# Optimization experiments

Measured on AMD Instinct MI355X. Metric: run time of the kernel, lower is better.

Reference implementation:

```python
import jax, jax.numpy as jnp
import numpy as np

B, T, D = 1, 2048, 4096
H, G = 32, 8
HD = D // H          # 128
REP = H // G         # 4
KV_DIM = 2 * HD * G  # 2048


def setup_inputs() -> dict:
    key = jax.random.key(0)
    k0, k1, k2, k3 = jax.random.split(key, 4)
    x = jax.random.normal(k0, (B, T, D), dtype=jnp.float32)
    Wq = jax.random.normal(k1, (D, D), dtype=jnp.float32) * 0.02
    Wkv = jax.random.normal(k2, (D, KV_DIM), dtype=jnp.float32) * 0.02
    Wo = jax.random.normal(k3, (D, D), dtype=jnp.float32) * 0.02
    bo = jnp.zeros((D,), dtype=jnp.float32)
    return {"x": x, "Wq": Wq, "Wkv": Wkv, "Wo": Wo, "bo": bo}


def reference(x, Wq, Wkv, Wo, bo):
    b, t, d = x.shape
    # projections (qkv_bias=False)
    q = jnp.dot(x, Wq).reshape(b, t, H, HD).transpose(0, 2, 1, 3)        # (b,H,t,hd)
    kv = jnp.dot(x, Wkv).reshape(b, t, G, 2, HD).transpose(2, 3, 0, 1, 4)  # (G,2,b,t,hd)
    k, v = kv[:, 0], kv[:, 1]                                             # (G,b,t,hd)
    # faithful to torch: unsqueeze+repeat then flat view(b, H, t, hd)
    k = jnp.broadcast_to(k[:, :, None], (G, b, REP, t, HD)).reshape(b, H, t, HD)
    v = jnp.broadcast_to(v[:, :, None], (G, b, REP, t, HD)).reshape(b, H, t, HD)
    # attention: mask then scale, matching original order
    scores = jnp.einsum('bhqd,bhkd->bhqk', q, k)                          # (b,H,t,t)
    causal = jnp.triu(jnp.ones((t, t), dtype=bool), 1)
    scores = jnp.where(causal[None, None], -jnp.inf, scores)
    weights = jax.nn.softmax(scores * (1.0 / HD ** 0.5), axis=-1)
    ctx = jnp.einsum('bhqk,bhkd->bhqd', weights, v)                       # (b,H,t,hd)
    ctx = ctx.transpose(0, 2, 1, 3).reshape(b, t, d)
    return jnp.dot(ctx, Wo) + bo
```

## Files before the change

### kernel.cpp

```cpp
#include <hip/hip_runtime.h>

#define T_SEQ 2048
#define D_MODEL 4096
#define NH 32
#define NG 8
#define HD 128

typedef unsigned short u16;
typedef __bf16 bf16x8 __attribute__((ext_vector_type(8)));
typedef float f32x4 __attribute__((ext_vector_type(4)));

#define AS1 __attribute__((address_space(1)))
#define AS3 __attribute__((address_space(3)))

__device__ __forceinline__ void async_cp16(const u16* g, u16* l) {
  __builtin_amdgcn_global_load_lds((AS1 void*)g, (AS3 void*)l, 16, 0, 0);
}

__device__ __forceinline__ u16 f2bf(float f){
  union { float f; unsigned x; } v; v.f = f;
  unsigned r = v.x + 0x7FFFu + ((v.x >> 16) & 1u);
  return (u16)(r >> 16);
}

__global__ __launch_bounds__(256) void cvt_k(const float* __restrict__ in,
                                             u16* __restrict__ out, int n4)
{
  int i = blockIdx.x * 256 + threadIdx.x;
  if (i >= n4) return;
  float4 v = *(const float4*)&in[(size_t)i * 4];
  short4 o;
  o.x = (short)f2bf(v.x); o.y = (short)f2bf(v.y);
  o.z = (short)f2bf(v.z); o.w = (short)f2bf(v.w);
  *(short4*)&out[(size_t)i * 4] = o;
}

__global__ __launch_bounds__(256) void transpose_k(const float* __restrict__ in,
                                                   u16* __restrict__ out, int R, int C)
{
  __shared__ __align__(16) u16 tile[32][36];
  int c0 = blockIdx.x * 32, r0 = blockIdx.y * 32;
  int t = threadIdx.x;
  int lr = t >> 3, lc = (t & 7) * 4;
  float4 v4 = *(const float4*)&in[(size_t)(r0 + lr) * C + c0 + lc];
  tile[lr][lc + 0] = f2bf(v4.x);
  tile[lr][lc + 1] = f2bf(v4.y);
  tile[lr][lc + 2] = f2bf(v4.z);
  tile[lr][lc + 3] = f2bf(v4.w);
  __syncthreads();
  short4 v;
  v.x = (short)tile[lc + 0][lr];
  v.y = (short)tile[lc + 1][lr];
  v.z = (short)tile[lc + 2][lr];
  v.w = (short)tile[lc + 3][lr];
  *(short4*)&out[(size_t)(c0 + lr) * R + r0 + lc] = v;
}

template<int MODE>
__global__ __launch_bounds__(256) void gemm_k(
    const u16* __restrict__ A, const u16* __restrict__ BT,
    u16* __restrict__ Cout, u16* __restrict__ Kout, u16* __restrict__ Vout,
    float* __restrict__ Fout, const float* __restrict__ bias, int K, int N)
{
  __shared__ __align__(16) u16 sA[2 * 128 * 64];
  __shared__ __align__(16) u16 sB[2 * 128 * 64];
  const int t = threadIdx.x;
  const int lane = t & 63, wave = t >> 6;
  const int quad = lane >> 4, lm = lane & 15;
  const int wm = wave >> 1, wn = wave & 1;
  const int m0 = blockIdx.y * 128, n0 = blockIdx.x * 128;
  const int ntk = K >> 6;
  const f32x4 fzero = {0.f, 0.f, 0.f, 0.f};

  const int sr_sub = lane >> 3;
  const int sgl = (lane & 7) ^ sr_sub;

  f32x4 acc[4][4];
  #pragma unroll
  for (int i = 0; i < 4; i++)
    #pragma unroll
    for (int j = 0; j < 4; j++) acc[i][j] = fzero;

  auto stage = [&](int td) {
    const int k0 = td << 6;
    u16* dA = sA + (td & 1) * (128 * 64);
    u16* dB = sB + (td & 1) * (128 * 64);
    #pragma unroll
    for (int c = 0; c < 4; c++) {
      int r = c * 32 + wave * 8 + sr_sub;
      async_cp16(&A [(size_t)(m0 + r) * K + k0 + sgl * 8], &dA[(c * 256 + wave * 64) * 8]);
      async_cp16(&BT[(size_t)(n0 + r) * K + k0 + sgl * 8], &dB[(c * 256 + wave * 64) * 8]);
    }
  };

  stage(0);
  stage(1);

  for (int ti = 0; ti < ntk; ++ti) {
    if (ti + 1 < ntk) { asm volatile("s_waitcnt vmcnt(8)" ::: "memory"); }
    else             { asm volatile("s_waitcnt vmcnt(0)" ::: "memory"); }
    __builtin_amdgcn_s_barrier();
    asm volatile("" ::: "memory");

    const u16* cA = sA + (ti & 1) * (128 * 64);
    const u16* cB = sB + (ti & 1) * (128 * 64);

    __builtin_amdgcn_s_setprio(1);
    #pragma unroll
    for (int kb = 0; kb < 2; kb++) {
      bf16x8 af[4], bfr[4];
      #pragma unroll
      for (int mt = 0; mt < 4; mt++) {
        int row = wm * 64 + mt * 16 + lm;
        af[mt] = *(const bf16x8*)&cA[row * 64 + (((kb * 4 + quad) ^ (lm & 7)) * 8)];
      }
      #pragma unroll
      for (int nt = 0; nt < 4; nt++) {
        int row = wn * 64 + nt * 16 + lm;
        bfr[nt] = *(const bf16x8*)&cB[row * 64 + (((kb * 4 + quad) ^ (lm & 7)) * 8)];
      }
      #pragma unroll
      for (int mt = 0; mt < 4; mt++)
        #pragma unroll
        for (int nt = 0; nt < 4; nt++)
          acc[mt][nt] = __builtin_amdgcn_mfma_f32_16x16x32_bf16(af[mt], bfr[nt], acc[mt][nt], 0, 0, 0);
    }
    __builtin_amdgcn_s_setprio(0);

    __builtin_amdgcn_s_barrier();
    asm volatile("" ::: "memory");
    if (ti + 2 < ntk) stage(ti + 2);
  }

  #pragma unroll
  for (int mt = 0; mt < 4; mt++) {
    #pragma unroll
    for (int nt = 0; nt < 4; nt++) {
      int gcol = n0 + wn * 64 + nt * 16 + lm;
      int grow0 = m0 + wm * 64 + mt * 16 + quad * 4;
      if (MODE == 0) {
        #pragma unroll
        for (int r = 0; r < 4; r++)
          Cout[(size_t)(grow0 + r) * N + gcol] = f2bf(acc[mt][nt][r]);
      } else if (MODE == 1) {
        int g = gcol >> 8, s = (gcol >> 7) & 1, hd = gcol & 127;
        if (s) {
          short4 pv;
          pv.x = (short)f2bf(acc[mt][nt][0]);
          pv.y = (short)f2bf(acc[mt][nt][1]);
          pv.z = (short)f2bf(acc[mt][nt][2]);
          pv.w = (short)f2bf(acc[mt][nt][3]);
          *(short4*)&Vout[((size_t)g * HD + hd) * T_SEQ + grow0] = pv;
        } else {
          #pragma unroll
          for (int r = 0; r < 4; r++)
            Kout[((size_t)g * T_SEQ + grow0 + r) * HD + hd] = f2bf(acc[mt][nt][r]);
        }
      } else {
        #pragma unroll
        for (int r = 0; r < 4; r++)
          Fout[(size_t)(grow0 + r) * N + gcol] = acc[mt][nt][r] + bias[gcol];
      }
    }
  }
}

__global__ __launch_bounds__(256) void attn_k(
    const u16* __restrict__ Q, const u16* __restrict__ Kb,
    const u16* __restrict__ Vt, u16* __restrict__ ctx)
{
  __shared__ __align__(16) u16 sK[2 * 64 * 128];
  __shared__ __align__(16) u16 sV[2 * 128 * 64];
  __shared__ __align__(16) u16 sP[4 * 16 * 72];
  const int t = threadIdx.x;
  const int lane = t & 63, wave = t >> 6;
  const int quad = lane >> 4, lm = lane & 15;

  const int id = blockIdx.x + gridDim.x * blockIdx.y;
  const int g = id & 7;
  const int idx = id >> 3;
  const int h = g * 4 + (idx & 3);
  const int q0 = (31 - (idx >> 2)) * 64;
  const int nt = (q0 >> 6) + 1;

  const float scale = 0.088388347648318447f;
  const float C1 = scale * 1.4426950408889634f;
  const float C2 = -14.0f * 1.4426950408889634f;
  const f32x4 fzero = {0.f, 0.f, 0.f, 0.f};

  bf16x8 aq[4];
  {
    const u16* qp = Q + (size_t)(q0 + wave * 16 + lm) * D_MODEL + h * HD + quad * 8;
    #pragma unroll
    for (int kb = 0; kb < 4; kb++) aq[kb] = *(const bf16x8*)(qp + kb * 32);
  }
  bf16x8 bones;
  #pragma unroll
  for (int i = 0; i < 8; i++) bones[i] = (__bf16)1.0f;

  f32x4 o[8];
  #pragma unroll
  for (int i = 0; i < 8; i++) o[i] = fzero;
  f32x4 lacc = fzero;

  const u16* Kg = Kb + (size_t)g * T_SEQ * HD;
  const u16* Vg = Vt + (size_t)g * HD * T_SEQ;
  u16* sPw = sP + wave * 16 * 72;

  const int k_r_sub = lane >> 4;
  const int v_r_sub = lane >> 3;
  const int v_gl = (lane & 7) ^ v_r_sub;

  auto stage = [&](int td) {
    const int kv0 = td << 6;
    u16* dK = sK + (td & 1) * (64 * 128);
    u16* dV = sV + (td & 1) * (128 * 64);
    #pragma unroll
    for (int c = 0; c < 4; c++) {
      int rk = c * 16 + wave * 4 + k_r_sub;
      int kgl = (lane & 15) ^ (rk & 7);
      async_cp16(&Kg[(size_t)(kv0 + rk) * HD + kgl * 8], &dK[(c * 256 + wave * 64) * 8]);
      int rv = c * 32 + wave * 8 + v_r_sub;
      async_cp16(&Vg[(size_t)rv * T_SEQ + kv0 + v_gl * 8], &dV[(c * 256 + wave * 64) * 8]);
    }
  };

  stage(0);
  if (nt > 1) stage(1);

  for (int ti = 0; ti < nt; ++ti) {
    if (ti + 1 < nt) { asm volatile("s_waitcnt vmcnt(8)" ::: "memory"); }
    else             { asm volatile("s_waitcnt vmcnt(0)" ::: "memory"); }
    __builtin_amdgcn_s_barrier();
    asm volatile("" ::: "memory");

    const u16* cK = sK + (ti & 1) * (64 * 128);
    const u16* cV = sV + (ti & 1) * (128 * 64);
    const int kv0 = ti << 6;

    f32x4 s[4];
    __builtin_amdgcn_s_setprio(1);
    #pragma unroll
    for (int nt4 = 0; nt4 < 4; nt4++) {
      s[nt4] = fzero;
      #pragma unroll
      for (int kb = 0; kb < 4; kb++) {
        int row = nt4 * 16 + lm;
        bf16x8 bk = *(const bf16x8*)&cK[row * 128 + (((kb * 4 + quad) ^ (lm & 7)) * 8)];
        s[nt4] = __builtin_amdgcn_mfma_f32_16x16x32_bf16(aq[kb], bk, s[nt4], 0, 0, 0);
      }
    }
    __builtin_amdgcn_s_setprio(0);

    if (ti == nt - 1) {
      #pragma unroll
      for (int r = 0; r < 4; r++) {
        int qr = q0 + wave * 16 + quad * 4 + r;
        #pragma unroll
        for (int nt4 = 0; nt4 < 4; nt4++) {
          int kvc = kv0 + nt4 * 16 + lm;
          float p = exp2f(fmaf(s[nt4][r], C1, C2));
          p = (kvc > qr) ? 0.f : p;
          sPw[(quad * 4 + r) * 72 + nt4 * 16 + lm] = f2bf(p);
        }
      }
    } else {
      #pragma unroll
      for (int r = 0; r < 4; r++) {
        #pragma unroll
        for (int nt4 = 0; nt4 < 4; nt4++) {
          float p = exp2f(fmaf(s[nt4][r], C1, C2));
          sPw[(quad * 4 + r) * 72 + nt4 * 16 + lm] = f2bf(p);
        }
      }
    }

    __builtin_amdgcn_s_setprio(1);
    #pragma unroll
    for (int kb2 = 0; kb2 < 2; kb2++) {
      bf16x8 ap = *(const bf16x8*)&sPw[lm * 72 + kb2 * 32 + quad * 8];
      lacc = __builtin_amdgcn_mfma_f32_16x16x32_bf16(ap, bones, lacc, 0, 0, 0);
      #pragma unroll
      for (int n8 = 0; n8 < 8; n8++) {
        int row = n8 * 16 + lm;
        bf16x8 bv = *(const bf16x8*)&cV[row * 64 + (((kb2 * 4 + quad) ^ (lm & 7)) * 8)];
        o[n8] = __builtin_amdgcn_mfma_f32_16x16x32_bf16(ap, bv, o[n8], 0, 0, 0);
      }
    }
    __builtin_amdgcn_s_setprio(0);

    __builtin_amdgcn_s_barrier();
    asm volatile("" ::: "memory");
    if (ti + 2 < nt) stage(ti + 2);
  }

  #pragma unroll
  for (int r = 0; r < 4; r++) {
    float inv = 1.f / lacc[r];
    #pragma unroll
    for (int n8 = 0; n8 < 8; n8++) {
      ctx[(size_t)(q0 + wave * 16 + quad * 4 + r) * D_MODEL + h * HD + n8 * 16 + lm]
          = f2bf(o[n8][r] * inv);
    }
  }
}

extern "C" void kernel_launch(void* const* d_in, const int* in_sizes, int n_in,
                              void* d_out, int out_size, void* d_ws, size_t ws_size,
                              hipStream_t stream)
{
  const float* x   = (const float*)d_in[0];
  const float* Wq  = (const float*)d_in[1];
  const float* Wkv = (const float*)d_in[2];
  const float* Wo  = (const float*)d_in[3];
  const float* bo  = (const float*)d_in[4];
  float* out = (float*)d_out;

  char* ws = (char*)d_ws;
  const size_t SZ_T   = 33554432;
  const size_t SZ_ACT = 16777216;
  const size_t SZ_KV  = 4194304;
  u16* Tb = (u16*)(ws);
  u16* Xb = (u16*)(ws + SZ_T);
  u16* Qb = (u16*)(ws + SZ_T + SZ_ACT);
  u16* Kb = (u16*)(ws + SZ_T + 2 * SZ_ACT);
  u16* Vt = (u16*)(ws + SZ_T + 2 * SZ_ACT + SZ_KV);
  u16* Cx = Xb;

  cvt_k<<<dim3(8192, 1, 1), 256, 0, stream>>>(x, Xb, 2097152);
  transpose_k<<<dim3(128, 128, 1), 256, 0, stream>>>(Wq, Tb, 4096, 4096);
  gemm_k<0><<<dim3(32, 16, 1), 256, 0, stream>>>(Xb, Tb, Qb, nullptr, nullptr, nullptr, nullptr, 4096, 4096);
  transpose_k<<<dim3(64, 128, 1), 256, 0, stream>>>(Wkv, Tb, 4096, 2048);
  gemm_k<1><<<dim3(16, 16, 1), 256, 0, stream>>>(Xb, Tb, nullptr, Kb, Vt, nullptr, nullptr, 4096, 2048);
  attn_k<<<dim3(32, 32, 1), 256, 0, stream>>>(Qb, Kb, Vt, Cx);
  transpose_k<<<dim3(128, 128, 1), 256, 0, stream>>>(Wo, Tb, 4096, 4096);
  gemm_k<2><<<dim3(32, 16, 1), 256, 0, stream>>>(Cx, Tb, nullptr, nullptr, nullptr, out, bo, 4096, 4096);
}
```

Before: 481.5 us.

## Double attention query tile to 128 rows per block for K/V reuse

```diff
diff --git a/kernel.cpp b/kernel.cpp
--- a/kernel.cpp
+++ b/kernel.cpp
@@ -171,41 +171,45 @@
 {
   __shared__ __align__(16) u16 sK[2 * 64 * 128];
   __shared__ __align__(16) u16 sV[2 * 128 * 64];
-  __shared__ __align__(16) u16 sP[4 * 16 * 72];
+  __shared__ __align__(16) u16 sP[4 * 32 * 64];
   const int t = threadIdx.x;
   const int lane = t & 63, wave = t >> 6;
   const int quad = lane >> 4, lm = lane & 15;
 
-  const int id = blockIdx.x + gridDim.x * blockIdx.y;
+  const int id = blockIdx.x;
   const int g = id & 7;
-  const int idx = id >> 3;
-  const int h = g * 4 + (idx & 3);
-  const int q0 = (31 - (idx >> 2)) * 64;
-  const int nt = (q0 >> 6) + 1;
+  const int j = id >> 3;
+  const int h = g * 4 + (j & 3);
+  const int qpos = j >> 2;
+  const int q0 = (qpos < 8 ? 15 - qpos : qpos - 8) * 128;
+  const int nt = (q0 >> 6) + 2;
 
   const float scale = 0.088388347648318447f;
   const float C1 = scale * 1.4426950408889634f;
   const float C2 = -14.0f * 1.4426950408889634f;
   const f32x4 fzero = {0.f, 0.f, 0.f, 0.f};
 
-  bf16x8 aq[4];
+  bf16x8 aq0[4], aq1[4];
   {
-    const u16* qp = Q + (size_t)(q0 + wave * 16 + lm) * D_MODEL + h * HD + quad * 8;
-    #pragma unroll
-    for (int kb = 0; kb < 4; kb++) aq[kb] = *(const bf16x8*)(qp + kb * 32);
+    const u16* qp = Q + (size_t)(q0 + wave * 32 + lm) * D_MODEL + h * HD + quad * 8;
+    #pragma unroll
+    for (int kb = 0; kb < 4; kb++) {
+      aq0[kb] = *(const bf16x8*)(qp + kb * 32);
+      aq1[kb] = *(const bf16x8*)(qp + (size_t)16 * D_MODEL + kb * 32);
+    }
   }
   bf16x8 bones;
   #pragma unroll
   for (int i = 0; i < 8; i++) bones[i] = (__bf16)1.0f;
 
-  f32x4 o[8];
-  #pragma unroll
-  for (int i = 0; i < 8; i++) o[i] = fzero;
-  f32x4 lacc = fzero;
+  f32x4 o0[8], o1[8];
+  #pragma unroll
+  for (int i = 0; i < 8; i++) { o0[i] = fzero; o1[i] = fzero; }
+  f32x4 lacc0 = fzero, lacc1 = fzero;
 
   const u16* Kg = Kb + (size_t)g * T_SEQ * HD;
   const u16* Vg = Vt + (size_t)g * HD * T_SEQ;
-  u16* sPw = sP + wave * 16 * 72;
+  u16* sPw = sP + wave * 32 * 64;
 
   const int k_r_sub = lane >> 4;
   const int v_r_sub = lane >> 3;
@@ -226,7 +230,7 @@
   };
 
   stage(0);
-  if (nt > 1) stage(1);
+  stage(1);
 
   for (int ti = 0; ti < nt; ++ti) {
     if (ti + 1 < nt) { asm volatile("s_waitcnt vmcnt(8)" ::: "memory"); }
@@ -238,39 +242,51 @@
     const u16* cV = sV + (ti & 1) * (128 * 64);
     const int kv0 = ti << 6;
 
-    f32x4 s[4];
+    f32x4 s0[4], s1[4];
     __builtin_amdgcn_s_setprio(1);
     #pragma unroll
     for (int nt4 = 0; nt4 < 4; nt4++) {
-      s[nt4] = fzero;
+      s0[nt4] = fzero; s1[nt4] = fzero;
       #pragma unroll
       for (int kb = 0; kb < 4; kb++) {
         int row = nt4 * 16 + lm;
         bf16x8 bk = *(const bf16x8*)&cK[row * 128 + (((kb * 4 + quad) ^ (lm & 7)) * 8)];
-        s[nt4] = __builtin_amdgcn_mfma_f32_16x16x32_bf16(aq[kb], bk, s[nt4], 0, 0, 0);
+        s0[nt4] = __builtin_amdgcn_mfma_f32_16x16x32_bf16(aq0[kb], bk, s0[nt4], 0, 0, 0);
+        s1[nt4] = __builtin_amdgcn_mfma_f32_16x16x32_bf16(aq1[kb], bk, s1[nt4], 0, 0, 0);
       }
     }
     __builtin_amdgcn_s_setprio(0);
 
-    if (ti == nt - 1) {
-      #pragma unroll
-      for (int r = 0; r < 4; r++) {
-        int qr = q0 + wave * 16 + quad * 4 + r;
-        #pragma unroll
-        for (int nt4 = 0; nt4 < 4; nt4++) {
-          int kvc = kv0 + nt4 * 16 + lm;
-          float p = exp2f(fmaf(s[nt4][r], C1, C2));
-          p = (kvc > qr) ? 0.f : p;
-          sPw[(quad * 4 + r) * 72 + nt4 * 16 + lm] = f2bf(p);
+    const int wrow0 = quad * 4;
+    if (ti >= nt - 2) {
+      #pragma unroll
+      for (int gq = 0; gq < 2; gq++) {
+        #pragma unroll
+        for (int r = 0; r < 4; r++) {
+          int row = gq * 16 + wrow0 + r;
+          int qr = q0 + wave * 32 + row;
+          #pragma unroll
+          for (int nt4 = 0; nt4 < 4; nt4++) {
+            int kvc = kv0 + nt4 * 16 + lm;
+            float sv = gq ? s1[nt4][r] : s0[nt4][r];
+            float p = exp2f(fmaf(sv, C1, C2));
+            p = (kvc > qr) ? 0.f : p;
+            sPw[row * 64 + (((nt4 * 2 + (lm >> 3)) ^ (row & 7)) * 8) + (lm & 7)] = f2bf(p);
+          }
         }
       }
     } else {
       #pragma unroll
-      for (int r = 0; r < 4; r++) {
-        #pragma unroll
-        for (int nt4 = 0; nt4 < 4; nt4++) {
-          float p = exp2f(fmaf(s[nt4][r], C1, C2));
-          sPw[(quad * 4 + r) * 72 + nt4 * 16 + lm] = f2bf(p);
+      for (int gq = 0; gq < 2; gq++) {
+        #pragma unroll
+        for (int r = 0; r < 4; r++) {
+          int row = gq * 16 + wrow0 + r;
+          #pragma unroll
+          for (int nt4 = 0; nt4 < 4; nt4++) {
+            float sv = gq ? s1[nt4][r] : s0[nt4][r];
+            float p = exp2f(fmaf(sv, C1, C2));
+            sPw[row * 64 + (((nt4 * 2 + (lm >> 3)) ^ (row & 7)) * 8) + (lm & 7)] = f2bf(p);
+          }
         }
       }
     }
@@ -278,13 +294,17 @@
     __builtin_amdgcn_s_setprio(1);
     #pragma unroll
     for (int kb2 = 0; kb2 < 2; kb2++) {
-      bf16x8 ap = *(const bf16x8*)&sPw[lm * 72 + kb2 * 32 + quad * 8];
-      lacc = __builtin_amdgcn_mfma_f32_16x16x32_bf16(ap, bones, lacc, 0, 0, 0);
+      int r0w = lm, r1w = 16 + lm;
+      bf16x8 ap0 = *(const bf16x8*)&sPw[r0w * 64 + (((kb2 * 4 + quad) ^ (r0w & 7)) * 8)];
+      bf16x8 ap1 = *(const bf16x8*)&sPw[r1w * 64 + (((kb2 * 4 + quad) ^ (r1w & 7)) * 8)];
+      lacc0 = __builtin_amdgcn_mfma_f32_16x16x32_bf16(ap0, bones, lacc0, 0, 0, 0);
+      lacc1 = __builtin_amdgcn_mfma_f32_16x16x32_bf16(ap1, bones, lacc1, 0, 0, 0);
       #pragma unroll
       for (int n8 = 0; n8 < 8; n8++) {
         int row = n8 * 16 + lm;
         bf16x8 bv = *(const bf16x8*)&cV[row * 64 + (((kb2 * 4 + quad) ^ (lm & 7)) * 8)];
-        o[n8] = __builtin_amdgcn_mfma_f32_16x16x32_bf16(ap, bv, o[n8], 0, 0, 0);
+        o0[n8] = __builtin_amdgcn_mfma_f32_16x16x32_bf16(ap0, bv, o0[n8], 0, 0, 0);
+        o1[n8] = __builtin_amdgcn_mfma_f32_16x16x32_bf16(ap1, bv, o1[n8], 0, 0, 0);
       }
     }
     __builtin_amdgcn_s_setprio(0);
@@ -296,11 +316,14 @@
 
   #pragma unroll
   for (int r = 0; r < 4; r++) {
-    float inv = 1.f / lacc[r];
+    float inv0 = 1.f / lacc0[r];
+    float inv1 = 1.f / lacc1[r];
     #pragma unroll
     for (int n8 = 0; n8 < 8; n8++) {
-      ctx[(size_t)(q0 + wave * 16 + quad * 4 + r) * D_MODEL + h * HD + n8 * 16 + lm]
-          = f2bf(o[n8][r] * inv);
+      ctx[(size_t)(q0 + wave * 32 + quad * 4 + r) * D_MODEL + h * HD + n8 * 16 + lm]
+          = f2bf(o0[n8][r] * inv0);
+      ctx[(size_t)(q0 + wave * 32 + 16 + quad * 4 + r) * D_MODEL + h * HD + n8 * 16 + lm]
+          = f2bf(o1[n8][r] * inv1);
     }
   }
 }
@@ -332,7 +355,7 @@
   gemm_k<0><<<dim3(32, 16, 1), 256, 0, stream>>>(Xb, Tb, Qb, nullptr, nullptr, nullptr, nullptr, 4096, 4096);
   transpose_k<<<dim3(64, 128, 1), 256, 0, stream>>>(Wkv, Tb, 4096, 2048);
   gemm_k<1><<<dim3(16, 16, 1), 256, 0, stream>>>(Xb, Tb, nullptr, Kb, Vt, nullptr, nullptr, 4096, 2048);
-  attn_k<<<dim3(32, 32, 1), 256, 0, stream>>>(Qb, Kb, Vt, Cx);
+  attn_k<<<dim3(512, 1, 1), 256, 0, stream>>>(Qb, Kb, Vt, Cx);
   transpose_k<<<dim3(128, 128, 1), 256, 0, stream>>>(Wo, Tb, 4096, 4096);
   gemm_k<2><<<dim3(32, 16, 1), 256, 0, stream>>>(Cx, Tb, nullptr, nullptr, nullptr, out, bo, 4096, 4096);
 }
```

Result: slower. 492.1 us (+2.2%).
